# Optimization experiments

Hardware: AMD Instinct MI355X
Metric: run time of the kernel (lower is better)

Reference implementation:

```python
import jax, jax.numpy as jnp
from jax import lax
import numpy as np

T, B, NIN = 512, 512, 64
H1, H2, H3 = 100, 50, 25


def lstm_layer(x, w_ih, w_hh, b_ih, b_hh):
    # x: [T, B, in]; torch gate order (i, f, g, o); weights [4H, in]/[4H, H]
    H = w_hh.shape[1]
    xg = jnp.einsum('tbi,gi->tbg', x, w_ih) + b_ih + b_hh  # [T, B, 4H]

    def step(carry, xg_t):
        h, c = carry
        g = xg_t + h @ w_hh.T
        i, f, gg, o = jnp.split(g, 4, axis=-1)
        c = jax.nn.sigmoid(f) * c + jax.nn.sigmoid(i) * jnp.tanh(gg)
        h = jax.nn.sigmoid(o) * jnp.tanh(c)
        return (h, c), h

    h0 = jnp.zeros((x.shape[1], H), x.dtype)
    _, hs = lax.scan(step, (h0, h0), xg)
    return hs  # [T, B, H]


def setup_inputs() -> dict:
    key = jax.random.key(0)
    ks = jax.random.split(key, 16)
    s = 0.1  # init scale for stability
    return {
        'x': jax.random.normal(ks[0], (T, B, NIN), jnp.float32),
        'w_ih1': jax.random.normal(ks[1], (4 * H1, NIN), jnp.float32) * s,
        'w_hh1': jax.random.normal(ks[2], (4 * H1, H1), jnp.float32) * s,
        'b_ih1': jax.random.normal(ks[3], (4 * H1,), jnp.float32) * s,
        'b_hh1': jax.random.normal(ks[4], (4 * H1,), jnp.float32) * s,
        'w_ih2': jax.random.normal(ks[5], (4 * H2, H1), jnp.float32) * s,
        'w_hh2': jax.random.normal(ks[6], (4 * H2, H2), jnp.float32) * s,
        'b_ih2': jax.random.normal(ks[7], (4 * H2,), jnp.float32) * s,
        'b_hh2': jax.random.normal(ks[8], (4 * H2,), jnp.float32) * s,
        'w_ih3': jax.random.normal(ks[9], (4 * H3, H2), jnp.float32) * s,
        'w_hh3': jax.random.normal(ks[10], (4 * H3, H3), jnp.float32) * s,
        'b_ih3': jax.random.normal(ks[11], (4 * H3,), jnp.float32) * s,
        'b_hh3': jax.random.normal(ks[12], (4 * H3,), jnp.float32) * s,
        'w_lin': jax.random.normal(ks[13], (1, H3), jnp.float32) * s,
        'b_lin': jax.random.normal(ks[14], (1,), jnp.float32) * s,
    }


def reference(x, w_ih1, w_hh1, b_ih1, b_hh1,
              w_ih2, w_hh2, b_ih2, b_hh2,
              w_ih3, w_hh3, b_ih3, b_hh3,
              w_lin, b_lin):
    # Dropout layers are identity at inference.
    h = lstm_layer(x, w_ih1, w_hh1, b_ih1, b_hh1)
    h = lstm_layer(h, w_ih2, w_hh2, b_ih2, b_hh2)
    h = lstm_layer(h, w_ih3, w_hh3, b_ih3, b_hh3)
    return h @ w_lin.T + b_lin  # [T, B, 1]
```

## Files before the change

kernel.cpp:

```cpp
#include <hip/hip_runtime.h>
#include <math.h>

#define T_STEPS 512
#define BATCH   512

__device__ __forceinline__ float sigmoidf_(float x) {
    return 1.0f / (1.0f + __expf(-x));
}
__device__ __forceinline__ float tanhf_(float x) {
    float ax = fabsf(x);
    float e  = __expf(-2.0f * ax);
    float t  = (1.0f - e) / (1.0f + e);
    return copysignf(t, x);
}

__global__ __launch_bounds__(448, 1) void lstm1_kernel(
    const float* __restrict__ x,
    const float* __restrict__ w_ih,
    const float* __restrict__ w_hh,
    const float* __restrict__ b_ih, const float* __restrict__ b_hh,
    float* __restrict__ h1out)
{
    __shared__ __align__(16) float xs[2][2][64];
    __shared__ __align__(16) float hs[2][104];
    __shared__ __align__(16) float gs[2][400];

    const int tid = threadIdx.x;
    const int b0  = blockIdx.x * 2;

    float wih[64], whh[100], bias = 0.0f;
    if (tid < 400) {
        bias = b_ih[tid] + b_hh[tid];
        #pragma unroll
        for (int k = 0; k < 64; ++k)  wih[k] = w_ih[tid * 64 + k];
        #pragma unroll
        for (int k = 0; k < 100; ++k) whh[k] = w_hh[tid * 100 + k];
    }

    if (tid < 128) xs[0][tid >> 6][tid & 63] = x[(size_t)b0 * 64 + tid];
    if (tid < 200) hs[tid / 100][tid % 100] = 0.0f;
    const int ub = (tid < 200) ? tid / 100 : 0;
    const int uu = (tid < 200) ? tid % 100 : 0;
    float c = 0.0f;
    __syncthreads();

    for (int t = 0; t < T_STEPS; ++t) {
        const int cur = t & 1, nxt = cur ^ 1;
        float pre = 0.0f;
        if (tid < 128 && t + 1 < T_STEPS)
            pre = x[((size_t)(t + 1) * BATCH + b0) * 64 + tid];
        if (tid < 400) {
            float a00 = bias, a01 = 0.0f, a10 = bias, a11 = 0.0f;
            const float4* xa = (const float4*)xs[cur][0];
            const float4* xb = (const float4*)xs[cur][1];
            #pragma unroll
            for (int k = 0; k < 16; ++k) {
                float4 va = xa[k], vb = xb[k];
                a00 = fmaf(va.x, wih[4*k+0], a00); a10 = fmaf(vb.x, wih[4*k+0], a10);
                a01 = fmaf(va.y, wih[4*k+1], a01); a11 = fmaf(vb.y, wih[4*k+1], a11);
                a00 = fmaf(va.z, wih[4*k+2], a00); a10 = fmaf(vb.z, wih[4*k+2], a10);
                a01 = fmaf(va.w, wih[4*k+3], a01); a11 = fmaf(vb.w, wih[4*k+3], a11);
            }
            const float4* h0 = (const float4*)hs[0];
            const float4* h1 = (const float4*)hs[1];
            #pragma unroll
            for (int k = 0; k < 25; ++k) {
                float4 v0 = h0[k], v1 = h1[k];
                a00 = fmaf(v0.x, whh[4*k+0], a00); a10 = fmaf(v1.x, whh[4*k+0], a10);
                a01 = fmaf(v0.y, whh[4*k+1], a01); a11 = fmaf(v1.y, whh[4*k+1], a11);
                a00 = fmaf(v0.z, whh[4*k+2], a00); a10 = fmaf(v1.z, whh[4*k+2], a10);
                a01 = fmaf(v0.w, whh[4*k+3], a01); a11 = fmaf(v1.w, whh[4*k+3], a11);
            }
            gs[0][tid] = a00 + a01;
            gs[1][tid] = a10 + a11;
        }
        __syncthreads();
        if (tid < 128 && t + 1 < T_STEPS) xs[nxt][tid >> 6][tid & 63] = pre;
        if (tid < 200) {
            float gi = gs[ub][uu],       gf = gs[ub][100 + uu];
            float gg = gs[ub][200 + uu], go = gs[ub][300 + uu];
            c = sigmoidf_(gf) * c + sigmoidf_(gi) * tanhf_(gg);
            float h = sigmoidf_(go) * tanhf_(c);
            hs[ub][uu] = h;
            h1out[((size_t)t * BATCH + b0 + ub) * 100 + uu] = h;
        }
        __syncthreads();
    }
}

__global__ __launch_bounds__(512, 1) void lstm23_kernel(
    const float* __restrict__ h1g,
    const float* __restrict__ w_ih2, const float* __restrict__ w_hh2,
    const float* __restrict__ b_ih2, const float* __restrict__ b_hh2,
    const float* __restrict__ w_ih3, const float* __restrict__ w_hh3,
    const float* __restrict__ b_ih3, const float* __restrict__ b_hh3,
    const float* __restrict__ w_lin, const float* __restrict__ b_lin,
    float* __restrict__ out)
{
    __shared__ __align__(16) float xs2[2][2][112];
    __shared__ __align__(16) float h2s[2][56];
    __shared__ __align__(16) float g2 [2][200];
    __shared__ __align__(16) float x3b[2][2][56];
    __shared__ __align__(16) float h3s[2][28];
    __shared__ __align__(16) float g3 [2][100];
    __shared__ __align__(16) float h3o[2][2][28];

    const int tid = threadIdx.x;
    const int b0  = blockIdx.x * 2;

    float wa[100], wb[50], bias = 0.0f;
    int bb = 0, u3 = 0;
    if (tid < 200) {
        bias = b_ih2[tid] + b_hh2[tid];
        #pragma unroll
        for (int k = 0; k < 100; ++k) wa[k] = w_ih2[tid * 100 + k];
        #pragma unroll
        for (int k = 0; k < 50; ++k)  wb[k] = w_hh2[tid * 50 + k];
    } else if (tid >= 256 && tid < 456) {
        int q = tid - 256; bb = q / 100; u3 = q % 100;
        bias = b_ih3[u3] + b_hh3[u3];
        #pragma unroll
        for (int k = 0; k < 50; ++k) wa[k] = w_ih3[u3 * 50 + k];
        #pragma unroll
        for (int k = 0; k < 25; ++k) wb[k] = w_hh3[u3 * 25 + k];
    } else if (tid >= 456 && tid < 458) {
        bias = b_lin[0];
        #pragma unroll
        for (int k = 0; k < 25; ++k) wa[k] = w_lin[k];
    }

    const int b2  = (tid < 100) ? tid / 50 : 0;
    const int u2  = (tid < 100) ? tid % 50 : 0;
    const int q3  = (tid >= 256 && tid < 306) ? (tid - 256) : 0;
    const int b3  = q3 / 25, u3u = q3 % 25;
    float c2 = 0.0f, c3 = 0.0f;

    if (tid < 200) xs2[0][tid / 100][tid % 100] = h1g[(size_t)b0 * 100 + tid];
    if (tid < 100) h2s[tid / 50][tid % 50] = 0.0f;
    if (tid >= 100 && tid < 150) { int q = tid - 100; h3s[q / 25][q % 25] = 0.0f; }
    __syncthreads();

    for (int it = 0; it < T_STEPS + 2; ++it) {
        float pre = 0.0f;
        if (tid < 200 && it + 1 < T_STEPS)
            pre = h1g[((size_t)(it + 1) * BATCH + b0) * 100 + tid];

        if (tid < 200 && it < T_STEPS) {
            const int cur = it & 1;
            float a00 = bias, a01 = 0.0f, a10 = bias, a11 = 0.0f;
            const float4* xa = (const float4*)xs2[cur][0];
            const float4* xb = (const float4*)xs2[cur][1];
            #pragma unroll
            for (int k = 0; k < 25; ++k) {
                float4 va = xa[k], vb = xb[k];
                a00 = fmaf(va.x, wa[4*k+0], a00); a10 = fmaf(vb.x, wa[4*k+0], a10);
                a01 = fmaf(va.y, wa[4*k+1], a01); a11 = fmaf(vb.y, wa[4*k+1], a11);
                a00 = fmaf(va.z, wa[4*k+2], a00); a10 = fmaf(vb.z, wa[4*k+2], a10);
                a01 = fmaf(va.w, wa[4*k+3], a01); a11 = fmaf(vb.w, wa[4*k+3], a11);
            }
            const float2* h20 = (const float2*)h2s[0];
            const float2* h21 = (const float2*)h2s[1];
            #pragma unroll
            for (int k = 0; k < 25; ++k) {
                float2 v0 = h20[k], v1 = h21[k];
                a00 = fmaf(v0.x, wb[2*k+0], a00); a10 = fmaf(v1.x, wb[2*k+0], a10);
                a01 = fmaf(v0.y, wb[2*k+1], a01); a11 = fmaf(v1.y, wb[2*k+1], a11);
            }
            g2[0][tid] = a00 + a01;
            g2[1][tid] = a10 + a11;
        }

        if (tid >= 256 && tid < 456 && it >= 1 && it <= T_STEPS) {
            const int s3 = it - 1;
            float a0 = bias, a1 = 0.0f;
            const float2* xv = (const float2*)x3b[s3 & 1][bb];
            #pragma unroll
            for (int k = 0; k < 25; ++k) {
                float2 v = xv[k];
                a0 = fmaf(v.x, wa[2*k+0], a0);
                a1 = fmaf(v.y, wa[2*k+1], a1);
            }
            #pragma unroll
            for (int k = 0; k < 25; ++k)
                a0 = fmaf(h3s[bb][k], wb[k], a0);
            g3[bb][u3] = a0 + a1;
        }

        if (tid >= 456 && tid < 458 && it >= 2) {
            const int sl = it - 2;
            const int lb = tid - 456;
            float o = bias;
            #pragma unroll
            for (int k = 0; k < 25; ++k)
                o = fmaf(h3o[sl & 1][lb][k], wa[k], o);
            out[(size_t)sl * BATCH + b0 + lb] = o;
        }
        __syncthreads();

        if (tid < 200 && it + 1 < T_STEPS)
            xs2[(it + 1) & 1][tid / 100][tid % 100] = pre;

        if (tid < 100 && it < T_STEPS) {
            float gi = g2[b2][u2],       gf = g2[b2][50 + u2];
            float gg = g2[b2][100 + u2], go = g2[b2][150 + u2];
            c2 = sigmoidf_(gf) * c2 + sigmoidf_(gi) * tanhf_(gg);
            float h = sigmoidf_(go) * tanhf_(c2);
            h2s[b2][u2] = h;
            x3b[it & 1][b2][u2] = h;
        }

        if (tid >= 256 && tid < 306 && it >= 1 && it <= T_STEPS) {
            const int s3 = it - 1;
            float gi = g3[b3][u3u],      gf = g3[b3][25 + u3u];
            float gg = g3[b3][50 + u3u], go = g3[b3][75 + u3u];
            c3 = sigmoidf_(gf) * c3 + sigmoidf_(gi) * tanhf_(gg);
            float h = sigmoidf_(go) * tanhf_(c3);
            h3s[b3][u3u] = h;
            h3o[s3 & 1][b3][u3u] = h;
        }
        __syncthreads();
    }
}

extern "C" void kernel_launch(void* const* d_in, const int* in_sizes, int n_in,
                              void* d_out, int out_size, void* d_ws, size_t ws_size,
                              hipStream_t stream)
{
    const float* x     = (const float*)d_in[0];
    const float* w_ih1 = (const float*)d_in[1];
    const float* w_hh1 = (const float*)d_in[2];
    const float* b_ih1 = (const float*)d_in[3];
    const float* b_hh1 = (const float*)d_in[4];
    const float* w_ih2 = (const float*)d_in[5];
    const float* w_hh2 = (const float*)d_in[6];
    const float* b_ih2 = (const float*)d_in[7];
    const float* b_hh2 = (const float*)d_in[8];
    const float* w_ih3 = (const float*)d_in[9];
    const float* w_hh3 = (const float*)d_in[10];
    const float* b_ih3 = (const float*)d_in[11];
    const float* b_hh3 = (const float*)d_in[12];
    const float* w_lin = (const float*)d_in[13];
    const float* b_lin = (const float*)d_in[14];
    float* out = (float*)d_out;

    const size_t h1_bytes = (size_t)T_STEPS * BATCH * 100 * sizeof(float);
    if (ws_size < h1_bytes) return;

    float* h1 = (float*)d_ws;

    lstm1_kernel<<<BATCH / 2, 448, 0, stream>>>(x, w_ih1, w_hh1, b_ih1, b_hh1, h1);
    lstm23_kernel<<<BATCH / 2, 512, 0, stream>>>(h1,
                                                 w_ih2, w_hh2, b_ih2, b_hh2,
                                                 w_ih3, w_hh3, b_ih3, b_hh3,
                                                 w_lin, b_lin, out);
}
```

Baseline: 1.619 ms.

## Hoist input projections into chunked GEMMs and run scans with one batch row per block

Input-to-hidden projections for layers 1 and 2 are moved out of the recurrent loop into separate parallel GEMM kernels over time chunks, and the recurrent scans now use one batch row per block with 512 blocks instead of 256. State is carried between chunks through the workspace. The aim is to shorten the serial per-step critical path and use more compute units. The cost is extra global traffic for the precomputed gates, plus many kernel launches across chunks.

After: 2.210 ms. 36.5% more time.

```diff
diff --git a/kernel.cpp b/kernel.cpp
--- a/kernel.cpp
+++ b/kernel.cpp
@@ -14,211 +14,260 @@
     return copysignf(t, x);
 }
 
-__global__ __launch_bounds__(448, 1) void lstm1_kernel(
-    const float* __restrict__ x,
-    const float* __restrict__ w_ih,
+template<int K, int N, int NT>
+__global__ __launch_bounds__(NT, 1) void xg_gemm_kernel(
+    const float* __restrict__ A,
+    const float* __restrict__ W,
+    const float* __restrict__ bih, const float* __restrict__ bhh,
+    float* __restrict__ xg)
+{
+    __shared__ __align__(16) float As[64 * K];
+    const int tid = threadIdx.x;
+
+    float w[K];
+    float bias = 0.0f;
+    if (tid < N) {
+        bias = bih[tid] + bhh[tid];
+        #pragma unroll
+        for (int k = 0; k < K; ++k) w[k] = W[tid * K + k];
+    }
+
+    const size_t r0 = (size_t)blockIdx.x * 64;
+    const float4* Ag = (const float4*)(A + r0 * K);
+    float4* As4 = (float4*)As;
+    for (int i = tid; i < 64 * K / 4; i += NT) As4[i] = Ag[i];
+    __syncthreads();
+
+    if (tid < N) {
+        for (int r = 0; r < 64; ++r) {
+            const float4* a4 = (const float4*)(As + r * K);
+            float acc0 = bias, acc1 = 0.0f;
+            #pragma unroll
+            for (int k4 = 0; k4 < K / 4; ++k4) {
+                float4 v = a4[k4];
+                acc0 = fmaf(v.x, w[4*k4+0], acc0);
+                acc1 = fmaf(v.y, w[4*k4+1], acc1);
+                acc0 = fmaf(v.z, w[4*k4+2], acc0);
+                acc1 = fmaf(v.w, w[4*k4+3], acc1);
+            }
+            xg[(r0 + r) * N + tid] = acc0 + acc1;
+        }
+    }
+}
+
+__global__ __launch_bounds__(448, 1) void scan1_kernel(
+    const float* __restrict__ xg,
     const float* __restrict__ w_hh,
-    const float* __restrict__ b_ih, const float* __restrict__ b_hh,
-    float* __restrict__ h1out)
+    float* __restrict__ h1c,
+    float* __restrict__ c1state,
+    int t0, int CH)
 {
-    __shared__ __align__(16) float xs[2][2][64];
-    __shared__ __align__(16) float hs[2][104];
-    __shared__ __align__(16) float gs[2][400];
-
-    const int tid = threadIdx.x;
-    const int b0  = blockIdx.x * 2;
-
-    float wih[64], whh[100], bias = 0.0f;
+    __shared__ __align__(16) float h_s[100];
+    __shared__ __align__(16) float g_s[400];
+
+    const int tid  = threadIdx.x;
+    const int brow = blockIdx.x;
+
+    float w[100];
     if (tid < 400) {
-        bias = b_ih[tid] + b_hh[tid];
-        #pragma unroll
-        for (int k = 0; k < 64; ++k)  wih[k] = w_ih[tid * 64 + k];
-        #pragma unroll
-        for (int k = 0; k < 100; ++k) whh[k] = w_hh[tid * 100 + k];
-    }
-
-    if (tid < 128) xs[0][tid >> 6][tid & 63] = x[(size_t)b0 * 64 + tid];
-    if (tid < 200) hs[tid / 100][tid % 100] = 0.0f;
-    const int ub = (tid < 200) ? tid / 100 : 0;
-    const int uu = (tid < 200) ? tid % 100 : 0;
+        #pragma unroll
+        for (int k = 0; k < 100; ++k) w[k] = w_hh[tid * 100 + k];
+    }
+
     float c = 0.0f;
+    if (tid < 100) {
+        if (t0 == 0) {
+            h_s[tid] = 0.0f;
+        } else {
+            h_s[tid] = h1c[((size_t)(CH - 1) * BATCH + brow) * 100 + tid];
+            c        = c1state[(size_t)brow * 100 + tid];
+        }
+    }
+    float xgv = (tid < 400) ? xg[(size_t)brow * 400 + tid] : 0.0f;
     __syncthreads();
 
-    for (int t = 0; t < T_STEPS; ++t) {
-        const int cur = t & 1, nxt = cur ^ 1;
-        float pre = 0.0f;
-        if (tid < 128 && t + 1 < T_STEPS)
-            pre = x[((size_t)(t + 1) * BATCH + b0) * 64 + tid];
+    for (int tl = 0; tl < CH; ++tl) {
+        float pre = (tid < 400 && tl + 1 < CH)
+                  ? xg[((size_t)(tl + 1) * BATCH + brow) * 400 + tid] : 0.0f;
         if (tid < 400) {
-            float a00 = bias, a01 = 0.0f, a10 = bias, a11 = 0.0f;
-            const float4* xa = (const float4*)xs[cur][0];
-            const float4* xb = (const float4*)xs[cur][1];
-            #pragma unroll
-            for (int k = 0; k < 16; ++k) {
-                float4 va = xa[k], vb = xb[k];
-                a00 = fmaf(va.x, wih[4*k+0], a00); a10 = fmaf(vb.x, wih[4*k+0], a10);
-                a01 = fmaf(va.y, wih[4*k+1], a01); a11 = fmaf(vb.y, wih[4*k+1], a11);
-                a00 = fmaf(va.z, wih[4*k+2], a00); a10 = fmaf(vb.z, wih[4*k+2], a10);
-                a01 = fmaf(va.w, wih[4*k+3], a01); a11 = fmaf(vb.w, wih[4*k+3], a11);
-            }
-            const float4* h0 = (const float4*)hs[0];
-            const float4* h1 = (const float4*)hs[1];
-            #pragma unroll
-            for (int k = 0; k < 25; ++k) {
-                float4 v0 = h0[k], v1 = h1[k];
-                a00 = fmaf(v0.x, whh[4*k+0], a00); a10 = fmaf(v1.x, whh[4*k+0], a10);
-                a01 = fmaf(v0.y, whh[4*k+1], a01); a11 = fmaf(v1.y, whh[4*k+1], a11);
-                a00 = fmaf(v0.z, whh[4*k+2], a00); a10 = fmaf(v1.z, whh[4*k+2], a10);
-                a01 = fmaf(v0.w, whh[4*k+3], a01); a11 = fmaf(v1.w, whh[4*k+3], a11);
-            }
-            gs[0][tid] = a00 + a01;
-            gs[1][tid] = a10 + a11;
+            float a0 = xgv, a1 = 0.0f;
+            const float4* hv = (const float4*)h_s;
+            #pragma unroll
+            for (int k4 = 0; k4 < 25; ++k4) {
+                float4 v = hv[k4];
+                a0 = fmaf(v.x, w[4*k4+0], a0);
+                a1 = fmaf(v.y, w[4*k4+1], a1);
+                a0 = fmaf(v.z, w[4*k4+2], a0);
+                a1 = fmaf(v.w, w[4*k4+3], a1);
+            }
+            g_s[tid] = a0 + a1;
         }
         __syncthreads();
-        if (tid < 128 && t + 1 < T_STEPS) xs[nxt][tid >> 6][tid & 63] = pre;
-        if (tid < 200) {
-            float gi = gs[ub][uu],       gf = gs[ub][100 + uu];
-            float gg = gs[ub][200 + uu], go = gs[ub][300 + uu];
+        xgv = pre;
+        if (tid < 100) {
+            float gi = g_s[tid],       gf = g_s[100 + tid];
+            float gg = g_s[200 + tid], go = g_s[300 + tid];
             c = sigmoidf_(gf) * c + sigmoidf_(gi) * tanhf_(gg);
             float h = sigmoidf_(go) * tanhf_(c);
-            hs[ub][uu] = h;
-            h1out[((size_t)t * BATCH + b0 + ub) * 100 + uu] = h;
+            h_s[tid] = h;
+            h1c[((size_t)tl * BATCH + brow) * 100 + tid] = h;
         }
         __syncthreads();
     }
-}
-
-__global__ __launch_bounds__(512, 1) void lstm23_kernel(
-    const float* __restrict__ h1g,
-    const float* __restrict__ w_ih2, const float* __restrict__ w_hh2,
-    const float* __restrict__ b_ih2, const float* __restrict__ b_hh2,
-    const float* __restrict__ w_ih3, const float* __restrict__ w_hh3,
+    if (tid < 100) c1state[(size_t)brow * 100 + tid] = c;
+}
+
+__global__ __launch_bounds__(384, 1) void scan23_kernel(
+    const float* __restrict__ xg2,
+    const float* __restrict__ w_hh2,
+    const float* __restrict__ w_ih3,
+    const float* __restrict__ w_hh3,
     const float* __restrict__ b_ih3, const float* __restrict__ b_hh3,
     const float* __restrict__ w_lin, const float* __restrict__ b_lin,
-    float* __restrict__ out)
+    float* __restrict__ out,
+    float* __restrict__ h2state, float* __restrict__ c2state,
+    float* __restrict__ h3state, float* __restrict__ c3state,
+    int t0, int CH)
 {
-    __shared__ __align__(16) float xs2[2][2][112];
-    __shared__ __align__(16) float h2s[2][56];
-    __shared__ __align__(16) float g2 [2][200];
-    __shared__ __align__(16) float x3b[2][2][56];
-    __shared__ __align__(16) float h3s[2][28];
-    __shared__ __align__(16) float g3 [2][100];
-    __shared__ __align__(16) float h3o[2][2][28];
-
-    const int tid = threadIdx.x;
-    const int b0  = blockIdx.x * 2;
-
-    float wa[100], wb[50], bias = 0.0f;
-    int bb = 0, u3 = 0;
+    __shared__ __align__(16) float h2_s[52];
+    __shared__ __align__(16) float x3_s[2][52];
+    __shared__ __align__(16) float h3_s[28];
+    __shared__ __align__(16) float h3o_s[2][28];
+    __shared__ __align__(16) float g2_s[200];
+    __shared__ __align__(16) float g3_s[100];
+
+    const int tid  = threadIdx.x;
+    const int brow = blockIdx.x;
+
+    float wa[52], wb[28], bias = 0.0f;
+    #pragma unroll
+    for (int k = 0; k < 52; ++k) wa[k] = 0.0f;
+    #pragma unroll
+    for (int k = 0; k < 28; ++k) wb[k] = 0.0f;
+
     if (tid < 200) {
-        bias = b_ih2[tid] + b_hh2[tid];
-        #pragma unroll
-        for (int k = 0; k < 100; ++k) wa[k] = w_ih2[tid * 100 + k];
-        #pragma unroll
-        for (int k = 0; k < 50; ++k)  wb[k] = w_hh2[tid * 50 + k];
-    } else if (tid >= 256 && tid < 456) {
-        int q = tid - 256; bb = q / 100; u3 = q % 100;
-        bias = b_ih3[u3] + b_hh3[u3];
-        #pragma unroll
-        for (int k = 0; k < 50; ++k) wa[k] = w_ih3[u3 * 50 + k];
-        #pragma unroll
-        for (int k = 0; k < 25; ++k) wb[k] = w_hh3[u3 * 25 + k];
-    } else if (tid >= 456 && tid < 458) {
+        #pragma unroll
+        for (int k = 0; k < 50; ++k) wa[k] = w_hh2[tid * 50 + k];
+    } else if (tid >= 256 && tid < 356) {
+        int j = tid - 256;
+        bias = b_ih3[j] + b_hh3[j];
+        #pragma unroll
+        for (int k = 0; k < 50; ++k) wa[k] = w_ih3[j * 50 + k];
+        #pragma unroll
+        for (int k = 0; k < 25; ++k) wb[k] = w_hh3[j * 25 + k];
+    } else if (tid == 370) {
         bias = b_lin[0];
         #pragma unroll
         for (int k = 0; k < 25; ++k) wa[k] = w_lin[k];
     }
 
-    const int b2  = (tid < 100) ? tid / 50 : 0;
-    const int u2  = (tid < 100) ? tid % 50 : 0;
-    const int q3  = (tid >= 256 && tid < 306) ? (tid - 256) : 0;
-    const int b3  = q3 / 25, u3u = q3 % 25;
     float c2 = 0.0f, c3 = 0.0f;
-
-    if (tid < 200) xs2[0][tid / 100][tid % 100] = h1g[(size_t)b0 * 100 + tid];
-    if (tid < 100) h2s[tid / 50][tid % 50] = 0.0f;
-    if (tid >= 100 && tid < 150) { int q = tid - 100; h3s[q / 25][q % 25] = 0.0f; }
+    if (tid < 52)  { h2_s[tid] = 0.0f; x3_s[0][tid] = 0.0f; x3_s[1][tid] = 0.0f; }
+    if (tid >= 52 && tid < 80)  h3_s[tid - 52] = 0.0f;
+    if (tid >= 80 && tid < 108) h3o_s[0][tid - 80] = 0.0f;
+    if (tid >= 108 && tid < 136) h3o_s[1][tid - 108] = 0.0f;
     __syncthreads();
-
-    for (int it = 0; it < T_STEPS + 2; ++it) {
-        float pre = 0.0f;
-        if (tid < 200 && it + 1 < T_STEPS)
-            pre = h1g[((size_t)(it + 1) * BATCH + b0) * 100 + tid];
-
-        if (tid < 200 && it < T_STEPS) {
-            const int cur = it & 1;
-            float a00 = bias, a01 = 0.0f, a10 = bias, a11 = 0.0f;
-            const float4* xa = (const float4*)xs2[cur][0];
-            const float4* xb = (const float4*)xs2[cur][1];
-            #pragma unroll
-            for (int k = 0; k < 25; ++k) {
-                float4 va = xa[k], vb = xb[k];
-                a00 = fmaf(va.x, wa[4*k+0], a00); a10 = fmaf(vb.x, wa[4*k+0], a10);
-                a01 = fmaf(va.y, wa[4*k+1], a01); a11 = fmaf(vb.y, wa[4*k+1], a11);
-                a00 = fmaf(va.z, wa[4*k+2], a00); a10 = fmaf(vb.z, wa[4*k+2], a10);
-                a01 = fmaf(va.w, wa[4*k+3], a01); a11 = fmaf(vb.w, wa[4*k+3], a11);
-            }
-            const float2* h20 = (const float2*)h2s[0];
-            const float2* h21 = (const float2*)h2s[1];
-            #pragma unroll
-            for (int k = 0; k < 25; ++k) {
-                float2 v0 = h20[k], v1 = h21[k];
-                a00 = fmaf(v0.x, wb[2*k+0], a00); a10 = fmaf(v1.x, wb[2*k+0], a10);
-                a01 = fmaf(v0.y, wb[2*k+1], a01); a11 = fmaf(v1.y, wb[2*k+1], a11);
-            }
-            g2[0][tid] = a00 + a01;
-            g2[1][tid] = a10 + a11;
-        }
-
-        if (tid >= 256 && tid < 456 && it >= 1 && it <= T_STEPS) {
-            const int s3 = it - 1;
+    if (t0 > 0) {
+        if (tid < 50) {
+            h2_s[tid] = h2state[(size_t)brow * 50 + tid];
+            c2        = c2state[(size_t)brow * 50 + tid];
+        }
+        if (tid >= 256 && tid < 281) {
+            int u = tid - 256;
+            h3_s[u] = h3state[(size_t)brow * 25 + u];
+            c3      = c3state[(size_t)brow * 25 + u];
+        }
+    }
+    float xgv = (tid < 200) ? xg2[(size_t)brow * 200 + tid] : 0.0f;
+    __syncthreads();
+
+    for (int it = 0; it < CH + 2; ++it) {
+        float pre = (tid < 200 && it + 1 < CH)
+                  ? xg2[((size_t)(it + 1) * BATCH + brow) * 200 + tid] : 0.0f;
+
+        if (tid < 200 && it < CH) {
+            float a0 = xgv, a1 = 0.0f;
+            const float4* hv = (const float4*)h2_s;
+            #pragma unroll
+            for (int k4 = 0; k4 < 13; ++k4) {
+                float4 v = hv[k4];
+                a0 = fmaf(v.x, wa[4*k4+0], a0);
+                a1 = fmaf(v.y, wa[4*k4+1], a1);
+                a0 = fmaf(v.z, wa[4*k4+2], a0);
+                a1 = fmaf(v.w, wa[4*k4+3], a1);
+            }
+            g2_s[tid] = a0 + a1;
+        }
+
+        if (tid >= 256 && tid < 356 && it >= 1 && it <= CH) {
             float a0 = bias, a1 = 0.0f;
-            const float2* xv = (const float2*)x3b[s3 & 1][bb];
-            #pragma unroll
-            for (int k = 0; k < 25; ++k) {
-                float2 v = xv[k];
-                a0 = fmaf(v.x, wa[2*k+0], a0);
-                a1 = fmaf(v.y, wa[2*k+1], a1);
-            }
-            #pragma unroll
-            for (int k = 0; k < 25; ++k)
-                a0 = fmaf(h3s[bb][k], wb[k], a0);
-            g3[bb][u3] = a0 + a1;
-        }
-
-        if (tid >= 456 && tid < 458 && it >= 2) {
-            const int sl = it - 2;
-            const int lb = tid - 456;
+            const float4* xv = (const float4*)x3_s[(it - 1) & 1];
+            #pragma unroll
+            for (int k4 = 0; k4 < 13; ++k4) {
+                float4 v = xv[k4];
+                a0 = fmaf(v.x, wa[4*k4+0], a0);
+                a1 = fmaf(v.y, wa[4*k4+1], a1);
+                a0 = fmaf(v.z, wa[4*k4+2], a0);
+                a1 = fmaf(v.w, wa[4*k4+3], a1);
+            }
+            const float4* hv = (const float4*)h3_s;
+            #pragma unroll
+            for (int k4 = 0; k4 < 7; ++k4) {
+                float4 v = hv[k4];
+                a0 = fmaf(v.x, wb[4*k4+0], a0);
+                a1 = fmaf(v.y, wb[4*k4+1], a1);
+                a0 = fmaf(v.z, wb[4*k4+2], a0);
+                a1 = fmaf(v.w, wb[4*k4+3], a1);
+            }
+            g3_s[tid - 256] = a0 + a1;
+        }
+
+        if (tid == 370 && it >= 2) {
             float o = bias;
-            #pragma unroll
-            for (int k = 0; k < 25; ++k)
-                o = fmaf(h3o[sl & 1][lb][k], wa[k], o);
-            out[(size_t)sl * BATCH + b0 + lb] = o;
+            const float4* hv = (const float4*)h3o_s[(it - 2) & 1];
+            #pragma unroll
+            for (int k4 = 0; k4 < 7; ++k4) {
+                float4 v = hv[k4];
+                o = fmaf(v.x, wa[4*k4+0], o);
+                o = fmaf(v.y, wa[4*k4+1], o);
+                o = fmaf(v.z, wa[4*k4+2], o);
+                o = fmaf(v.w, wa[4*k4+3], o);
+            }
+            out[(size_t)(t0 + it - 2) * BATCH + brow] = o;
         }
         __syncthreads();
 
-        if (tid < 200 && it + 1 < T_STEPS)
-            xs2[(it + 1) & 1][tid / 100][tid % 100] = pre;
-
-        if (tid < 100 && it < T_STEPS) {
-            float gi = g2[b2][u2],       gf = g2[b2][50 + u2];
-            float gg = g2[b2][100 + u2], go = g2[b2][150 + u2];
+        if (tid < 200) xgv = pre;
+
+        if (tid < 50 && it < CH) {
+            float gi = g2_s[tid],       gf = g2_s[50 + tid];
+            float gg = g2_s[100 + tid], go = g2_s[150 + tid];
             c2 = sigmoidf_(gf) * c2 + sigmoidf_(gi) * tanhf_(gg);
             float h = sigmoidf_(go) * tanhf_(c2);
-            h2s[b2][u2] = h;
-            x3b[it & 1][b2][u2] = h;
-        }
-
-        if (tid >= 256 && tid < 306 && it >= 1 && it <= T_STEPS) {
-            const int s3 = it - 1;
-            float gi = g3[b3][u3u],      gf = g3[b3][25 + u3u];
-            float gg = g3[b3][50 + u3u], go = g3[b3][75 + u3u];
+            h2_s[tid] = h;
+            x3_s[it & 1][tid] = h;
+        }
+
+        if (tid >= 256 && tid < 281 && it >= 1 && it <= CH) {
+            int u = tid - 256;
+            float gi = g3_s[u],      gf = g3_s[25 + u];
+            float gg = g3_s[50 + u], go = g3_s[75 + u];
             c3 = sigmoidf_(gf) * c3 + sigmoidf_(gi) * tanhf_(gg);
             float h = sigmoidf_(go) * tanhf_(c3);
-            h3s[b3][u3u] = h;
-            h3o[s3 & 1][b3][u3u] = h;
+            h3_s[u] = h;
+            h3o_s[(it - 1) & 1][u] = h;
         }
         __syncthreads();
+    }
+
+    if (tid < 50) {
+        h2state[(size_t)brow * 50 + tid] = h2_s[tid];
+        c2state[(size_t)brow * 50 + tid] = c2;
+    }
+    if (tid >= 256 && tid < 281) {
+        int u = tid - 256;
+        h3state[(size_t)brow * 25 + u] = h3_s[u];
+        c3state[(size_t)brow * 25 + u] = c3;
     }
 }
 
@@ -243,14 +292,34 @@
     const float* b_lin = (const float*)d_in[14];
     float* out = (float*)d_out;
 
-    const size_t h1_bytes = (size_t)T_STEPS * BATCH * 100 * sizeof(float);
-    if (ws_size < h1_bytes) return;
-
-    float* h1 = (float*)d_ws;
-
-    lstm1_kernel<<<BATCH / 2, 448, 0, stream>>>(x, w_ih1, w_hh1, b_ih1, b_hh1, h1);
-    lstm23_kernel<<<BATCH / 2, 512, 0, stream>>>(h1,
-                                                 w_ih2, w_hh2, b_ih2, b_hh2,
-                                                 w_ih3, w_hh3, b_ih3, b_hh3,
-                                                 w_lin, b_lin, out);
-}
+    const size_t state_bytes = (size_t)BATCH * (100 + 50 + 50 + 25 + 25) * sizeof(float);
+    int CH = 0;
+    for (int c = 128; c >= 8; c >>= 1) {
+        size_t need = (size_t)c * BATCH * 700 * sizeof(float) + state_bytes;
+        if (need <= ws_size) { CH = c; break; }
+    }
+    if (CH == 0) return;
+
+    char* ws = (char*)d_ws;
+    float* xg1c    = (float*)ws;
+    float* h1c     = xg1c + (size_t)CH * BATCH * 400;
+    float* xg2c    = h1c  + (size_t)CH * BATCH * 100;
+    float* c1state = xg2c + (size_t)CH * BATCH * 200;
+    float* h2state = c1state + (size_t)BATCH * 100;
+    float* c2state = h2state + (size_t)BATCH * 50;
+    float* h3state = c2state + (size_t)BATCH * 50;
+    float* c3state = h3state + (size_t)BATCH * 25;
+
+    const int rowtiles = CH * BATCH / 64;
+
+    for (int t0 = 0; t0 < T_STEPS; t0 += CH) {
+        xg_gemm_kernel<64, 400, 448><<<rowtiles, 448, 0, stream>>>(
+            x + (size_t)t0 * BATCH * 64, w_ih1, b_ih1, b_hh1, xg1c);
+        scan1_kernel<<<BATCH, 448, 0, stream>>>(xg1c, w_hh1, h1c, c1state, t0, CH);
+        xg_gemm_kernel<100, 200, 256><<<rowtiles, 256, 0, stream>>>(
+            h1c, w_ih2, b_ih2, b_hh2, xg2c);
+        scan23_kernel<<<BATCH, 384, 0, stream>>>(
+            xg2c, w_hh2, w_ih3, w_hh3, b_ih3, b_hh3, w_lin, b_lin, out,
+            h2state, c2state, h3state, c3state, t0, CH);
+    }
+}
```
